# Kernel tuning notes

Measured on AMD Instinct MI355X. Metric: run time of the kernel, lower is better.

Reference implementation:

```python
import jax, jax.numpy as jnp
import numpy as np

H = 16  # n_heads (from init_kwargs)


def l2norm(x, eps=1e-6):
    return x * jax.lax.rsqrt(jnp.sum(x * x, axis=-1, keepdims=True) + eps)


def causal_conv1d(x, w, b):
    # depthwise causal conv: x (B,T,D), w (D,k), b (D,). Matches torch
    # Conv1d(d,d,k,groups=d,padding=k-1) followed by [:, :, :T] truncation.
    T = x.shape[1]
    k = w.shape[1]
    xp = jnp.pad(x, ((0, 0), (k - 1, 0), (0, 0)))
    y = b
    for j in range(k):  # k=4 taps, fixed small loop
        y = y + xp[:, j:j + T, :] * w[:, j]
    return y


def setup_inputs():
    key = jax.random.key(0)
    ks = jax.random.split(key, 16)
    B, T, D, kc = 2, 2048, 1024, 4
    d = D // H
    s = 1.0 / np.sqrt(D)
    return {
        "x": jax.random.normal(ks[0], (B, T, D), jnp.float32),
        "Wq": jax.random.normal(ks[1], (D, D), jnp.float32) * s,
        "Wk": jax.random.normal(ks[2], (D, D), jnp.float32) * s,
        "Wv": jax.random.normal(ks[3], (D, D), jnp.float32) * s,
        "Wo": jax.random.normal(ks[4], (D, D), jnp.float32) * s,
        "Wg": jax.random.normal(ks[5], (D, D), jnp.float32) * s,
        "Wb": jax.random.normal(ks[6], (D, H), jnp.float32) * s,
        "cq_w": jax.random.normal(ks[7], (D, kc), jnp.float32) * 0.3,
        "cq_b": jax.random.normal(ks[8], (D,), jnp.float32) * 0.1,
        "ck_w": jax.random.normal(ks[9], (D, kc), jnp.float32) * 0.3,
        "ck_b": jax.random.normal(ks[10], (D,), jnp.float32) * 0.1,
        "cv_w": jax.random.normal(ks[11], (D, kc), jnp.float32) * 0.3,
        "cv_b": jax.random.normal(ks[12], (D,), jnp.float32) * 0.1,
        "nw": jnp.ones((d,), jnp.float32),
    }


def reference(x, Wq, Wk, Wv, Wo, Wg, Wb, cq_w, cq_b, ck_w, ck_b, cv_w, cv_b, nw):
    B, T, D = x.shape
    d = D // H
    q = l2norm(jax.nn.silu(causal_conv1d(x @ Wq, cq_w, cq_b)).reshape(B, T, H, d))
    q = q / jnp.sqrt(jnp.asarray(d, x.dtype))
    k = l2norm(jax.nn.silu(causal_conv1d(x @ Wk, ck_w, ck_b)).reshape(B, T, H, d))
    v = jax.nn.silu(causal_conv1d(x @ Wv, cv_w, cv_b)).reshape(B, T, H, d)
    gate = (x @ Wg).reshape(B, T, H, d)
    beta = jax.nn.sigmoid(x @ Wb)[..., None]  # (B,T,H,1)

    def step(S, qkvb):
        q_t, k_t, v_t, b_t = qkvb  # (B,H,d), (B,H,d), (B,H,d), (B,H,1)
        err = (v_t - jnp.einsum('bhk,bhkv->bhv', k_t, S)) * b_t
        S = S + jnp.einsum('bhk,bhv->bhkv', k_t, err)
        o_t = jnp.einsum('bhk,bhkv->bhv', q_t, S)
        return S, o_t

    S0 = jnp.zeros((B, H, d, d), x.dtype)
    xs = (q.transpose(1, 0, 2, 3), k.transpose(1, 0, 2, 3),
          v.transpose(1, 0, 2, 3), beta.transpose(1, 0, 2, 3))
    _, oT = jax.lax.scan(step, S0, xs)
    o = oT.transpose(1, 0, 2, 3)  # (B,T,H,d)
    # RMSNorm over head_dim
    o = o * jax.lax.rsqrt(jnp.mean(o * o, axis=-1, keepdims=True) + 1e-5) * nw
    o = o * jax.nn.silu(gate)
    return o.reshape(B, T, D) @ Wo
```

## Files before the change

### kernel.cpp

```cpp
#include <hip/hip_runtime.h>
#include <hip/hip_bf16.h>

typedef __attribute__((ext_vector_type(8))) short short8;
typedef __attribute__((ext_vector_type(4))) float f32x4;

#define TSEQ 2048
#define DMODEL 1024
#define NH 16
#define HD 64
#define PLANE 4194304

__device__ __forceinline__ ushort f2bf(float f) {
    union { float f; unsigned int u; } c; c.f = f;
    unsigned int u = c.u + 0x7fffu + ((c.u >> 16) & 1u);
    return (ushort)(u >> 16);
}

__device__ __forceinline__ float bf2f(ushort u) {
    union { unsigned int i; float f; } c; c.i = ((unsigned int)u) << 16;
    return c.f;
}

__device__ __forceinline__ void split2(float x, ushort& h, ushort& l) {
    h = f2bf(x);
    float r = x - bf2f(h);
    l = f2bf(r);
}

__device__ __forceinline__ float silu_f(float y) {
    return y / (1.f + __expf(-y));
}

__device__ __forceinline__ void gl_lds16(const float* g, float* l) {
    __builtin_amdgcn_global_load_lds(
        (__attribute__((address_space(1))) void*)g,
        (__attribute__((address_space(3))) void*)l, 16, 0, 0);
}
__device__ __forceinline__ void gl_lds16u(const ushort* g, ushort* l) {
    __builtin_amdgcn_global_load_lds(
        (__attribute__((address_space(1))) void*)g,
        (__attribute__((address_space(3))) void*)l, 16, 0, 0);
}

__global__ void gdn_cvt_x(const float* __restrict__ x, ushort* __restrict__ xb) {
    int i = blockIdx.x * 256 + threadIdx.x;
    float4 v = ((const float4*)x)[i];
    ushort4 o;
    o.x = f2bf(v.x); o.y = f2bf(v.y); o.z = f2bf(v.z); o.w = f2bf(v.w);
    ((ushort4*)xb)[i] = o;
}

__global__ void gdn_cvt_w(const float* __restrict__ Wq, const float* __restrict__ Wk,
                          const float* __restrict__ Wv, const float* __restrict__ Wg,
                          const float* __restrict__ Wo, ushort* __restrict__ wt) {
    __shared__ float tile[32][33];
    int z = blockIdx.z;
    const float* W = (z == 0) ? Wq : (z == 1) ? Wk : (z == 2) ? Wv : (z == 3) ? Wg : Wo;
    int n0 = blockIdx.x * 32, k0 = blockIdx.y * 32;
    int tx = threadIdx.x, ty = threadIdx.y;
    #pragma unroll
    for (int j = 0; j < 32; j += 8)
        tile[ty + j][tx] = W[(size_t)(k0 + ty + j) * DMODEL + n0 + tx];
    __syncthreads();
    ushort* o = wt + (size_t)z * DMODEL * DMODEL;
    #pragma unroll
    for (int j = 0; j < 32; j += 8)
        o[(size_t)(n0 + ty + j) * DMODEL + k0 + tx] = f2bf(tile[tx][ty + j]);
}

__global__ void gdn_beta(const float* __restrict__ x, const float* __restrict__ Wb,
                         float* __restrict__ betaT) {
    __shared__ float xs[16][DMODEL];
    int tid = threadIdx.x;
    int m0 = blockIdx.x * 16;
    #pragma unroll
    for (int i = 0; i < 16; i++) {
        int idx = i * 256 + tid;
        int row = idx >> 8, c4 = idx & 255;
        *(float4*)&xs[row][c4 * 4] =
            *(const float4*)&x[(size_t)(m0 + row) * DMODEL + c4 * 4];
    }
    __syncthreads();
    int h = tid & 15, mi = tid >> 4;
    float acc = 0.f;
    for (int k = 0; k < DMODEL; ++k)
        acc += xs[mi][k] * Wb[k * NH + h];
    int m = m0 + mi;
    int b = m >> 11, t = m & (TSEQ - 1);
    betaT[((b * NH + h) << 11) + t] = 1.f / (1.f + __expf(-acc));
}

#define BK 32
__global__ __launch_bounds__(256) void gdn_gemm(const ushort* __restrict__ A,
                                                const ushort* __restrict__ Bt,
                                                float* __restrict__ outF,
                                                size_t planeStride) {
    __shared__ ushort As[128 * BK];
    __shared__ ushort Bs[128 * BK];
    int tid = threadIdx.x;
    int lane = tid & 63, wid = tid >> 6;
    int wm = wid & 1, wn = wid >> 1;
    int l15 = lane & 15, quad = lane >> 4;
    int bm = blockIdx.x, bn = blockIdx.y;
    const int K = DMODEL;

    int e0 = wid, e1 = wid + 4;
    int srow0 = e0 * 16 + (lane >> 2), srow1 = e1 * 16 + (lane >> 2);
    int scol = (lane & 3) * 8;
    const ushort* Ag0 = A + (size_t)(bm * 128 + srow0) * K + scol;
    const ushort* Ag1 = A + (size_t)(bm * 128 + srow1) * K + scol;
    const ushort* Bg0 = Bt + (size_t)(bn * 128 + srow0) * K + scol;
    const ushort* Bg1 = Bt + (size_t)(bn * 128 + srow1) * K + scol;
    ushort* Al0 = As + e0 * 512;
    ushort* Al1 = As + e1 * 512;
    ushort* Bl0 = Bs + e0 * 512;
    ushort* Bl1 = Bs + e1 * 512;

    f32x4 acc[4][4];
    #pragma unroll
    for (int i = 0; i < 4; i++)
        #pragma unroll
        for (int j = 0; j < 4; j++)
            acc[i][j] = (f32x4){0.f, 0.f, 0.f, 0.f};

    for (int kt = 0; kt < K; kt += BK) {
        __syncthreads();
        gl_lds16u(Ag0 + kt, Al0);
        gl_lds16u(Ag1 + kt, Al1);
        gl_lds16u(Bg0 + kt, Bl0);
        gl_lds16u(Bg1 + kt, Bl1);
        __syncthreads();
        short8 af[4], bf[4];
        #pragma unroll
        for (int i = 0; i < 4; i++) {
            af[i] = *(const short8*)&As[(wm * 64 + i * 16 + l15) * BK + quad * 8];
            bf[i] = *(const short8*)&Bs[(wn * 64 + i * 16 + l15) * BK + quad * 8];
        }
        #pragma unroll
        for (int mt = 0; mt < 4; mt++)
            #pragma unroll
            for (int nt = 0; nt < 4; nt++)
                acc[mt][nt] = __builtin_amdgcn_mfma_f32_16x16x32_bf16(
                    af[mt], bf[nt], acc[mt][nt], 0, 0, 0);
    }

    #pragma unroll
    for (int mt = 0; mt < 4; mt++)
        #pragma unroll
        for (int nt = 0; nt < 4; nt++)
            #pragma unroll
            for (int r = 0; r < 4; r++) {
                int row = bm * 128 + wm * 64 + mt * 16 + quad * 4 + r;
                int col = bn * 128 + wn * 64 + nt * 16 + l15;
                outF[(size_t)(col >> 10) * planeStride + (size_t)row * 1024 + (col & 1023)]
                    = acc[mt][nt][r];
            }
}

__global__ __launch_bounds__(512, 2) void gdn_gemm256(const ushort* __restrict__ A,
                                                      const ushort* __restrict__ Bt,
                                                      float* __restrict__ outF,
                                                      size_t planeStride) {
    __shared__ ushort As[3][256 * BK];
    __shared__ ushort Bs[3][256 * BK];
    int tid = threadIdx.x;
    int lane = tid & 63, wid = tid >> 6;
    int wm = wid >> 2, wn = wid & 3;
    int l15 = lane & 15, quad = lane >> 4;
    int bm = blockIdx.x, bn = blockIdx.y;
    const int K = DMODEL;

    int e0 = wid * 2, e1 = wid * 2 + 1;
    int srow0 = e0 * 16 + (lane >> 2), srow1 = e1 * 16 + (lane >> 2);
    int scol = (lane & 3) * 8;
    const ushort* Ag0 = A + (size_t)(bm * 256 + srow0) * K + scol;
    const ushort* Ag1 = A + (size_t)(bm * 256 + srow1) * K + scol;
    const ushort* Bg0 = Bt + (size_t)(bn * 256 + srow0) * K + scol;
    const ushort* Bg1 = Bt + (size_t)(bn * 256 + srow1) * K + scol;

    f32x4 acc[8][4];
    #pragma unroll
    for (int i = 0; i < 8; i++)
        #pragma unroll
        for (int j = 0; j < 4; j++)
            acc[i][j] = (f32x4){0.f, 0.f, 0.f, 0.f};

    #pragma unroll
    for (int t = 0; t < 2; t++) {
        gl_lds16u(Ag0 + t * BK, &As[t][e0 * 512]);
        gl_lds16u(Ag1 + t * BK, &As[t][e1 * 512]);
        gl_lds16u(Bg0 + t * BK, &Bs[t][e0 * 512]);
        gl_lds16u(Bg1 + t * BK, &Bs[t][e1 * 512]);
    }
    asm volatile("s_waitcnt vmcnt(4)" ::: "memory");
    __builtin_amdgcn_s_barrier();

    #pragma unroll 1
    for (int c = 0; c < 32; ++c) {
        if (c + 2 < 32) {
            int s2 = (c + 2) % 3;
            int kt2 = (c + 2) * BK;
            gl_lds16u(Ag0 + kt2, &As[s2][e0 * 512]);
            gl_lds16u(Ag1 + kt2, &As[s2][e1 * 512]);
            gl_lds16u(Bg0 + kt2, &Bs[s2][e0 * 512]);
            gl_lds16u(Bg1 + kt2, &Bs[s2][e1 * 512]);
        }
        int cs = c % 3;
        short8 af[8], bf[4];
        #pragma unroll
        for (int mi = 0; mi < 8; mi++)
            af[mi] = *(const short8*)&As[cs][(wm * 128 + mi * 16 + l15) * BK + quad * 8];
        #pragma unroll
        for (int ni = 0; ni < 4; ni++)
            bf[ni] = *(const short8*)&Bs[cs][(wn * 64 + ni * 16 + l15) * BK + quad * 8];
        #pragma unroll
        for (int mi = 0; mi < 8; mi++)
            #pragma unroll
            for (int ni = 0; ni < 4; ni++)
                acc[mi][ni] = __builtin_amdgcn_mfma_f32_16x16x32_bf16(
                    af[mi], bf[ni], acc[mi][ni], 0, 0, 0);
        if (c < 30) {
            asm volatile("s_waitcnt vmcnt(4)" ::: "memory");
            __builtin_amdgcn_s_barrier();
        } else if (c == 30) {
            asm volatile("s_waitcnt vmcnt(0)" ::: "memory");
            __builtin_amdgcn_s_barrier();
        }
    }

    #pragma unroll
    for (int mi = 0; mi < 8; mi++)
        #pragma unroll
        for (int ni = 0; ni < 4; ni++)
            #pragma unroll
            for (int r = 0; r < 4; r++) {
                int row = bm * 256 + wm * 128 + mi * 16 + quad * 4 + r;
                int col = bn * 256 + wn * 64 + ni * 16 + l15;
                outF[(size_t)(col >> 10) * planeStride + (size_t)row * 1024 + (col & 1023)]
                    = acc[mi][ni][r];
            }
}

__global__ void gdn_conv(const float* __restrict__ pre,
                         const float* __restrict__ cqw, const float* __restrict__ cqb,
                         const float* __restrict__ ckw, const float* __restrict__ ckb,
                         const float* __restrict__ cvw, const float* __restrict__ cvb,
                         float* __restrict__ qn, float* __restrict__ kn, float* __restrict__ vn) {
    int m = blockIdx.x;
    int which = blockIdx.y;
    int t = m & (TSEQ - 1);
    const float* cw = (which == 0) ? cqw : (which == 1) ? ckw : cvw;
    const float* cb = (which == 0) ? cqb : (which == 1) ? ckb : cvb;
    float* dst = (which == 0) ? qn : (which == 1) ? kn : vn;
    int c = threadIdx.x * 4;

    float w[4][4];
    #pragma unroll
    for (int i = 0; i < 4; i++) {
        float4 t4 = ((const float4*)cw)[c + i];
        w[i][0] = t4.x; w[i][1] = t4.y; w[i][2] = t4.z; w[i][3] = t4.w;
    }
    float4 bias = ((const float4*)cb)[threadIdx.x];
    float y[4] = {bias.x, bias.y, bias.z, bias.w};

    const float* src = pre + (size_t)which * PLANE + (size_t)m * DMODEL + c;
    #pragma unroll
    for (int j = 0; j < 4; j++) {
        int tt = t - 3 + j;
        if (tt >= 0) {
            float4 xv = *(const float4*)(src + (long)(j - 3) * DMODEL);
            y[0] += xv.x * w[0][j];
            y[1] += xv.y * w[1][j];
            y[2] += xv.z * w[2][j];
            y[3] += xv.w * w[3][j];
        }
    }
    #pragma unroll
    for (int i = 0; i < 4; i++) y[i] = silu_f(y[i]);

    if (which < 2) {
        float ss = y[0]*y[0] + y[1]*y[1] + y[2]*y[2] + y[3]*y[3];
        ss += __shfl_xor(ss, 1);
        ss += __shfl_xor(ss, 2);
        ss += __shfl_xor(ss, 4);
        ss += __shfl_xor(ss, 8);
        float sc = rsqrtf(ss + 1e-6f);
        if (which == 0) sc *= 0.125f;
        #pragma unroll
        for (int i = 0; i < 4; i++) y[i] *= sc;
    }
    float4 o; o.x = y[0]; o.y = y[1]; o.z = y[2]; o.w = y[3];
    ((float4*)(dst + (size_t)m * 1024))[threadIdx.x] = o;
}

__global__ __launch_bounds__(256) void gdn_chunk(
    const float* __restrict__ kn, const float* __restrict__ vn,
    const float* __restrict__ betaT,
    ushort* __restrict__ WTst, ushort* __restrict__ U0st,
    float* __restrict__ Pst, float* __restrict__ Rst)
{
    __shared__ ushort Khi[64 * 72], Klo[64 * 72];
    __shared__ ushort KThi[64 * 72], KTlo[64 * 72];
    __shared__ ushort XThi[128 * 72], XTlo[128 * 72];
    __shared__ ushort Mneghi[64 * 72], Mneglo[64 * 72];
    __shared__ float  Xf[64 * 132];
    __shared__ float  MmDiag[4 * 16 * 20];
    __shared__ float  bet[64];

    int c = blockIdx.x, bh = blockIdx.y;
    int b = bh >> 4, h = bh & 15;
    int tid = threadIdx.x;
    int w = tid >> 6, lane = tid & 63;
    int l15 = lane & 15, quad = lane >> 4;
    size_t gbase = ((size_t)(b * TSEQ + c * 64)) * DMODEL + h * 64;
    size_t u = (size_t)bh * 32 + c;

    if (tid < 64) bet[tid] = betaT[((size_t)bh << 11) + c * 64 + tid];
    #pragma unroll
    for (int i = 0; i < 18; i++) {
        ((uint*)XThi)[tid + 256 * i] = 0u;
        ((uint*)XTlo)[tid + 256 * i] = 0u;
    }
    __syncthreads();

    #pragma unroll
    for (int i = 0; i < 4; i++) {
        int idx = tid + 256 * i;
        int r = idx >> 4, c4 = (idx & 15) * 4;
        float4 kv = *(const float4*)&kn[gbase + (size_t)r * DMODEL + c4];
        float4 vv = *(const float4*)&vn[gbase + (size_t)r * DMODEL + c4];
        float br = bet[r];
        float4 xk; xk.x = br * kv.x; xk.y = br * kv.y; xk.z = br * kv.z; xk.w = br * kv.w;
        float4 xv; xv.x = br * vv.x; xv.y = br * vv.y; xv.z = br * vv.z; xv.w = br * vv.w;
        *(float4*)&Xf[r * 132 + c4] = xk;
        *(float4*)&Xf[r * 132 + 64 + c4] = xv;
        ushort h0, l0, h1, l1, h2, l2, h3, l3;
        split2(kv.x, h0, l0); split2(kv.y, h1, l1);
        split2(kv.z, h2, l2); split2(kv.w, h3, l3);
        ((uint*)&Khi[r * 72 + c4])[0] = (uint)h0 | ((uint)h1 << 16);
        ((uint*)&Khi[r * 72 + c4])[1] = (uint)h2 | ((uint)h3 << 16);
        ((uint*)&Klo[r * 72 + c4])[0] = (uint)l0 | ((uint)l1 << 16);
        ((uint*)&Klo[r * 72 + c4])[1] = (uint)l2 | ((uint)l3 << 16);
        KThi[(c4 + 0) * 72 + r] = h0; KThi[(c4 + 1) * 72 + r] = h1;
        KThi[(c4 + 2) * 72 + r] = h2; KThi[(c4 + 3) * 72 + r] = h3;
        KTlo[(c4 + 0) * 72 + r] = l0; KTlo[(c4 + 1) * 72 + r] = l1;
        KTlo[(c4 + 2) * 72 + r] = l2; KTlo[(c4 + 3) * 72 + r] = l3;
    }
    __syncthreads();

    {
        f32x4 mAcc[4];
        #pragma unroll
        for (int tn = 0; tn < 4; tn++) mAcc[tn] = (f32x4){0.f, 0.f, 0.f, 0.f};
        #pragma unroll
        for (int ks = 0; ks < 2; ks++) {
            short8 aH = *(const short8*)&Khi[(16 * w + l15) * 72 + ks * 32 + quad * 8];
            short8 aL = *(const short8*)&Klo[(16 * w + l15) * 72 + ks * 32 + quad * 8];
            #pragma unroll
            for (int tn = 0; tn < 4; tn++) {
                short8 bH = *(const short8*)&Khi[(16 * tn + l15) * 72 + ks * 32 + quad * 8];
                short8 bL = *(const short8*)&Klo[(16 * tn + l15) * 72 + ks * 32 + quad * 8];
                mAcc[tn] = __builtin_amdgcn_mfma_f32_16x16x32_bf16(aH, bH, mAcc[tn], 0, 0, 0);
                mAcc[tn] = __builtin_amdgcn_mfma_f32_16x16x32_bf16(aH, bL, mAcc[tn], 0, 0, 0);
                mAcc[tn] = __builtin_amdgcn_mfma_f32_16x16x32_bf16(aL, bH, mAcc[tn], 0, 0, 0);
            }
        }
        #pragma unroll
        for (int tn = 0; tn < 4; tn++) {
            #pragma unroll
            for (int r = 0; r < 4; r++) {
                int row = 16 * w + quad * 4 + r;
                int col = tn * 16 + l15;
                float val = mAcc[tn][r] * bet[row];
                ushort hh = 0, ll = 0;
                if (col < row) {
                    float nv = -val;
                    hh = f2bf(nv);
                    ll = f2bf(nv - bf2f(hh));
                }
                Mneghi[row * 72 + col] = hh;
                Mneglo[row * 72 + col] = ll;
                if (tn == w) MmDiag[w * 320 + (row & 15) * 20 + l15] = val;
            }
        }
    }
    __syncthreads();

    #pragma unroll 1
    for (int st = 0; st < 4; st++) {
        int tb = st * 16;
        if (st) {
            f32x4 acc2[2];
            #pragma unroll
            for (int e = 0; e < 2; e++) {
                int tn = 2 * w + e;
                #pragma unroll
                for (int r = 0; r < 4; r++)
                    acc2[e][r] = Xf[(tb + quad * 4 + r) * 132 + tn * 16 + l15];
            }
            #pragma unroll
            for (int ks = 0; ks < 2; ks++) {
                short8 aH = *(const short8*)&Mneghi[(tb + l15) * 72 + ks * 32 + quad * 8];
                short8 aL = *(const short8*)&Mneglo[(tb + l15) * 72 + ks * 32 + quad * 8];
                #pragma unroll
                for (int e = 0; e < 2; e++) {
                    int tn = 2 * w + e;
                    short8 bH = *(const short8*)&XThi[(tn * 16 + l15) * 72 + ks * 32 + quad * 8];
                    short8 bL = *(const short8*)&XTlo[(tn * 16 + l15) * 72 + ks * 32 + quad * 8];
                    acc2[e] = __builtin_amdgcn_mfma_f32_16x16x32_bf16(aH, bH, acc2[e], 0, 0, 0);
                    acc2[e] = __builtin_amdgcn_mfma_f32_16x16x32_bf16(aH, bL, acc2[e], 0, 0, 0);
                    acc2[e] = __builtin_amdgcn_mfma_f32_16x16x32_bf16(aL, bH, acc2[e], 0, 0, 0);
                }
            }
            #pragma unroll
            for (int e = 0; e < 2; e++) {
                int tn = 2 * w + e;
                #pragma unroll
                for (int r = 0; r < 4; r++)
                    Xf[(tb + quad * 4 + r) * 132 + tn * 16 + l15] = acc2[e][r];
            }
        }
        __syncthreads();

        if (tid < 128) {
            const int j = tid;
            const float* MD = &MmDiag[st * 320];
            float xr[16];
            #pragma unroll
            for (int sb = 0; sb < 4; sb++) {
                float b4[4];
                #pragma unroll
                for (int i = 0; i < 4; i++)
                    b4[i] = Xf[(tb + sb * 4 + i) * 132 + j];
                #pragma unroll
                for (int u4 = 0; u4 < sb; u4++) {
                    #pragma unroll
                    for (int i = 0; i < 4; i++) {
                        float4 m4 = *(const float4*)&MD[(sb * 4 + i) * 20 + u4 * 4];
                        b4[i] -= m4.x * xr[u4 * 4 + 0] + m4.y * xr[u4 * 4 + 1]
                               + m4.z * xr[u4 * 4 + 2] + m4.w * xr[u4 * 4 + 3];
                    }
                }
                float x0 = b4[0];
                float x1 = b4[1] - MD[(sb * 4 + 1) * 20 + sb * 4 + 0] * x0;
                float x2 = b4[2] - MD[(sb * 4 + 2) * 20 + sb * 4 + 0] * x0
                                 - MD[(sb * 4 + 2) * 20 + sb * 4 + 1] * x1;
                float x3 = b4[3] - MD[(sb * 4 + 3) * 20 + sb * 4 + 0] * x0
                                 - MD[(sb * 4 + 3) * 20 + sb * 4 + 1] * x1
                                 - MD[(sb * 4 + 3) * 20 + sb * 4 + 2] * x2;
                xr[sb * 4 + 0] = x0; xr[sb * 4 + 1] = x1;
                xr[sb * 4 + 2] = x2; xr[sb * 4 + 3] = x3;
            }
            ushort hs[16], ls[16];
            #pragma unroll
            for (int i = 0; i < 16; i++) split2(xr[i], hs[i], ls[i]);
            uint4 ph0, ph1, pl0, pl1;
            ph0.x = (uint)hs[0] | ((uint)hs[1] << 16);  ph0.y = (uint)hs[2] | ((uint)hs[3] << 16);
            ph0.z = (uint)hs[4] | ((uint)hs[5] << 16);  ph0.w = (uint)hs[6] | ((uint)hs[7] << 16);
            ph1.x = (uint)hs[8] | ((uint)hs[9] << 16);  ph1.y = (uint)hs[10] | ((uint)hs[11] << 16);
            ph1.z = (uint)hs[12] | ((uint)hs[13] << 16); ph1.w = (uint)hs[14] | ((uint)hs[15] << 16);
            pl0.x = (uint)ls[0] | ((uint)ls[1] << 16);  pl0.y = (uint)ls[2] | ((uint)ls[3] << 16);
            pl0.z = (uint)ls[4] | ((uint)ls[5] << 16);  pl0.w = (uint)ls[6] | ((uint)ls[7] << 16);
            pl1.x = (uint)ls[8] | ((uint)ls[9] << 16);  pl1.y = (uint)ls[10] | ((uint)ls[11] << 16);
            pl1.z = (uint)ls[12] | ((uint)ls[13] << 16); pl1.w = (uint)ls[14] | ((uint)ls[15] << 16);
            *(uint4*)&XThi[j * 72 + tb] = ph0;  *(uint4*)&XThi[j * 72 + tb + 8] = ph1;
            *(uint4*)&XTlo[j * 72 + tb] = pl0;  *(uint4*)&XTlo[j * 72 + tb + 8] = pl1;
            if (j < 64) {
                ushort* wdst = WTst + u * 4096 + j * 64 + tb;
                *(uint4*)wdst = ph0; *(uint4*)(wdst + 8) = ph1;
            } else {
                ushort* udst = U0st + u * 4096 + (size_t)tb * 64 + (j - 64);
                #pragma unroll
                for (int i = 0; i < 16; i++) udst[i * 64] = hs[i];
            }
        }
        __syncthreads();
    }

    {
        f32x4 pAcc[4], rAcc[4];
        #pragma unroll
        for (int tn = 0; tn < 4; tn++) {
            pAcc[tn] = (f32x4){0.f, 0.f, 0.f, 0.f};
            rAcc[tn] = (f32x4){0.f, 0.f, 0.f, 0.f};
        }
        #pragma unroll
        for (int ks = 0; ks < 2; ks++) {
            short8 aH = *(const short8*)&XThi[(16 * w + l15) * 72 + ks * 32 + quad * 8];
            short8 aL = *(const short8*)&XTlo[(16 * w + l15) * 72 + ks * 32 + quad * 8];
            short8 cH = *(const short8*)&KThi[(16 * w + l15) * 72 + ks * 32 + quad * 8];
            short8 cL = *(const short8*)&KTlo[(16 * w + l15) * 72 + ks * 32 + quad * 8];
            #pragma unroll
            for (int tn = 0; tn < 4; tn++) {
                short8 bH = *(const short8*)&KThi[(16 * tn + l15) * 72 + ks * 32 + quad * 8];
                short8 bL = *(const short8*)&KTlo[(16 * tn + l15) * 72 + ks * 32 + quad * 8];
                pAcc[tn] = __builtin_amdgcn_mfma_f32_16x16x32_bf16(aH, bH, pAcc[tn], 0, 0, 0);
                pAcc[tn] = __builtin_amdgcn_mfma_f32_16x16x32_bf16(aH, bL, pAcc[tn], 0, 0, 0);
                pAcc[tn] = __builtin_amdgcn_mfma_f32_16x16x32_bf16(aL, bH, pAcc[tn], 0, 0, 0);
                short8 uH = *(const short8*)&XThi[(64 + 16 * tn + l15) * 72 + ks * 32 + quad * 8];
                short8 uL = *(const short8*)&XTlo[(64 + 16 * tn + l15) * 72 + ks * 32 + quad * 8];
                rAcc[tn] = __builtin_amdgcn_mfma_f32_16x16x32_bf16(cH, uH, rAcc[tn], 0, 0, 0);
                rAcc[tn] = __builtin_amdgcn_mfma_f32_16x16x32_bf16(cH, uL, rAcc[tn], 0, 0, 0);
                rAcc[tn] = __builtin_amdgcn_mfma_f32_16x16x32_bf16(cL, uH, rAcc[tn], 0, 0, 0);
            }
        }
        float* Po = Pst + u * 4096;
        float* Ro = Rst + u * 4096;
        #pragma unroll
        for (int tn = 0; tn < 4; tn++) {
            #pragma unroll
            for (int r = 0; r < 4; r++) {
                int row = 16 * w + quad * 4 + r;
                int col = tn * 16 + l15;
                Po[row * 64 + col] = pAcc[tn][r];
                Ro[col * 64 + row] = rAcc[tn][r];
            }
        }
    }
}

__global__ __launch_bounds__(256) void gdn_sstep(const float* __restrict__ Pst,
                                                 const float* __restrict__ Rst,
                                                 float* __restrict__ S0st)
{
    __shared__ float PTl[3][4096];
    __shared__ float Rl[3][1024];
    __shared__ float SshT[2][16][72];

    int bh = blockIdx.x >> 2, cg = blockIdx.x & 3;
    int tid = threadIdx.x;
    int t0 = (tid & 15) * 4;
    int j  = tid >> 4;
    int jg = cg * 16 + j;
    int wv = tid >> 6, ln = tid & 63;

    size_t ubase = (size_t)bh * 32 * 4096;

    *(float4*)&SshT[0][j][t0] = (float4){0.f, 0.f, 0.f, 0.f};

    #pragma unroll
    for (int t = 0; t < 2; t++) {
        size_t ub = ubase + (size_t)t * 4096;
        #pragma unroll
        for (int q = 0; q < 4; q++)
            gl_lds16(Pst + ub + (wv * 4 + q) * 256 + ln * 4, &PTl[t][(wv * 4 + q) * 256]);
        gl_lds16(Rst + ub + cg * 1024 + wv * 256 + ln * 4, &Rl[t][wv * 256]);
    }
    asm volatile("s_waitcnt vmcnt(5)" ::: "memory");
    asm volatile("s_waitcnt lgkmcnt(0)" ::: "memory");
    __builtin_amdgcn_s_barrier();

    int cur3 = 0;
    #pragma unroll 1
    for (int c = 0; c < 32; ++c) {
        int cur = c & 1, nxt = cur ^ 1;
        if (c + 2 < 32) {
            int b3 = cur3 + 2; if (b3 >= 3) b3 -= 3;
            size_t ub2 = ubase + (size_t)(c + 2) * 4096;
            #pragma unroll
            for (int q = 0; q < 4; q++)
                gl_lds16(Pst + ub2 + (wv * 4 + q) * 256 + ln * 4, &PTl[b3][(wv * 4 + q) * 256]);
            gl_lds16(Rst + ub2 + cg * 1024 + wv * 256 + ln * 4, &Rl[b3][wv * 256]);
        }
        float4 sold = *(const float4*)&SshT[cur][j][t0];
        size_t ub = ubase + (size_t)c * 4096;
        S0st[ub + (size_t)(t0 + 0) * 64 + jg] = sold.x;
        S0st[ub + (size_t)(t0 + 1) * 64 + jg] = sold.y;
        S0st[ub + (size_t)(t0 + 2) * 64 + jg] = sold.z;
        S0st[ub + (size_t)(t0 + 3) * 64 + jg] = sold.w;
        float4 racc = *(const float4*)&Rl[cur3][j * 64 + t0];
        float sub0 = 0.f, sub1 = 0.f, sub2 = 0.f, sub3 = 0.f;
        #pragma unroll
        for (int u4 = 0; u4 < 16; u4++) {
            float4 sv = *(const float4*)&SshT[cur][j][u4 * 4];
            #pragma unroll
            for (int e = 0; e < 4; e++) {
                float4 pt = *(const float4*)&PTl[cur3][(u4 * 4 + e) * 64 + t0];
                float s1 = (e == 0) ? sv.x : (e == 1) ? sv.y : (e == 2) ? sv.z : sv.w;
                sub0 = fmaf(pt.x, s1, sub0);
                sub1 = fmaf(pt.y, s1, sub1);
                sub2 = fmaf(pt.z, s1, sub2);
                sub3 = fmaf(pt.w, s1, sub3);
            }
        }
        float4 snew;
        snew.x = sold.x + racc.x - sub0;
        snew.y = sold.y + racc.y - sub1;
        snew.z = sold.z + racc.z - sub2;
        snew.w = sold.w + racc.w - sub3;
        *(float4*)&SshT[nxt][j][t0] = snew;
        if (c == 0)       { asm volatile("s_waitcnt vmcnt(9)"  ::: "memory"); }
        else if (c < 30)  { asm volatile("s_waitcnt vmcnt(13)" ::: "memory"); }
        else if (c == 30) { asm volatile("s_waitcnt vmcnt(8)"  ::: "memory"); }
        asm volatile("s_waitcnt lgkmcnt(0)" ::: "memory");
        __builtin_amdgcn_s_barrier();
        cur3 += 1; if (cur3 >= 3) cur3 -= 3;
    }
}

__global__ __launch_bounds__(256) void gdn_opass(
    const float* __restrict__ qn, const float* __restrict__ kn,
    const float* __restrict__ S0st, const ushort* __restrict__ WTst,
    const ushort* __restrict__ U0st, float* __restrict__ otmp2)
{
    __shared__ ushort pool[36864];
    ushort* Qhi  = pool;
    ushort* Qlo  = pool + 4608;
    ushort* Khi  = pool + 2 * 4608;
    ushort* Klo  = pool + 3 * 4608;
    ushort* SThi = pool + 4 * 4608;
    ushort* STlo = pool + 5 * 4608;
    ushort* Wn   = pool + 6 * 4608;
    ushort* Uu   = pool + 7 * 4608;
    ushort* Ghi  = Qhi;  ushort* Glo  = Qlo;
    ushort* EThi = Khi;  ushort* ETlo = Klo;

    int c = blockIdx.x, bh = blockIdx.y;
    int b = bh >> 4, h = bh & 15;
    int tid = threadIdx.x;
    int w = tid >> 6, lane = tid & 63;
    int l15 = lane & 15, quad = lane >> 4;
    size_t gbase = ((size_t)(b * TSEQ + c * 64)) * DMODEL + h * 64;
    size_t u = (size_t)bh * 32 + c;

    #pragma unroll
    for (int i = 0; i < 4; i++) {
        int idx = tid + 256 * i;
        int r = idx >> 4, c4 = (idx & 15) * 4;
        float4 qv = *(const float4*)&qn[gbase + (size_t)r * DMODEL + c4];
        float4 kv = *(const float4*)&kn[gbase + (size_t)r * DMODEL + c4];
        float4 sv = *(const float4*)&S0st[u * 4096 + (size_t)idx * 4];
        ushort h0, l0, h1, l1, h2, l2, h3, l3;
        split2(qv.x, h0, l0); split2(qv.y, h1, l1);
        split2(qv.z, h2, l2); split2(qv.w, h3, l3);
        ((uint*)&Qhi[r * 72 + c4])[0] = (uint)h0 | ((uint)h1 << 16);
        ((uint*)&Qhi[r * 72 + c4])[1] = (uint)h2 | ((uint)h3 << 16);
        ((uint*)&Qlo[r * 72 + c4])[0] = (uint)l0 | ((uint)l1 << 16);
        ((uint*)&Qlo[r * 72 + c4])[1] = (uint)l2 | ((uint)l3 << 16);
        split2(kv.x, h0, l0); split2(kv.y, h1, l1);
        split2(kv.z, h2, l2); split2(kv.w, h3, l3);
        ((uint*)&Khi[r * 72 + c4])[0] = (uint)h0 | ((uint)h1 << 16);
        ((uint*)&Khi[r * 72 + c4])[1] = (uint)h2 | ((uint)h3 << 16);
        ((uint*)&Klo[r * 72 + c4])[0] = (uint)l0 | ((uint)l1 << 16);
        ((uint*)&Klo[r * 72 + c4])[1] = (uint)l2 | ((uint)l3 << 16);
        split2(sv.x, h0, l0); split2(sv.y, h1, l1);
        split2(sv.z, h2, l2); split2(sv.w, h3, l3);
        SThi[(c4 + 0) * 72 + r] = h0; STlo[(c4 + 0) * 72 + r] = l0;
        SThi[(c4 + 1) * 72 + r] = h1; STlo[(c4 + 1) * 72 + r] = l1;
        SThi[(c4 + 2) * 72 + r] = h2; STlo[(c4 + 2) * 72 + r] = l2;
        SThi[(c4 + 3) * 72 + r] = h3; STlo[(c4 + 3) * 72 + r] = l3;
    }
    #pragma unroll
    for (int i = 0; i < 2; i++) {
        int idx = tid + 256 * i;
        uint4 w8 = ((const uint4*)(WTst + u * 4096))[idx];
        int ur = idx >> 3, t8 = (idx & 7) * 8;
        uint v0 = w8.x ^ 0x80008000u, v1 = w8.y ^ 0x80008000u;
        uint v2 = w8.z ^ 0x80008000u, v3 = w8.w ^ 0x80008000u;
        Wn[(t8 + 0) * 72 + ur] = (ushort)v0; Wn[(t8 + 1) * 72 + ur] = (ushort)(v0 >> 16);
        Wn[(t8 + 2) * 72 + ur] = (ushort)v1; Wn[(t8 + 3) * 72 + ur] = (ushort)(v1 >> 16);
        Wn[(t8 + 4) * 72 + ur] = (ushort)v2; Wn[(t8 + 5) * 72 + ur] = (ushort)(v2 >> 16);
        Wn[(t8 + 6) * 72 + ur] = (ushort)v3; Wn[(t8 + 7) * 72 + ur] = (ushort)(v3 >> 16);
        ((uint4*)Uu)[idx] = ((const uint4*)(U0st + u * 4096))[idx];
    }
    __syncthreads();

    f32x4 accG[4], accO[4], accE[4];
    #pragma unroll
    for (int tn = 0; tn < 4; tn++) {
        accG[tn] = (f32x4){0.f, 0.f, 0.f, 0.f};
        accO[tn] = (f32x4){0.f, 0.f, 0.f, 0.f};
        #pragma unroll
        for (int r = 0; r < 4; r++)
            accE[tn][r] = bf2f(Uu[(16 * w + quad * 4 + r) * 64 + tn * 16 + l15]);
    }
    #pragma unroll
    for (int ks = 0; ks < 2; ks++) {
        int ko = ks * 32 + quad * 8;
        short8 qH = *(const short8*)&Qhi[(16 * w + l15) * 72 + ko];
        short8 qL = *(const short8*)&Qlo[(16 * w + l15) * 72 + ko];
        short8 wA = *(const short8*)&Wn [(16 * w + l15) * 72 + ko];
        #pragma unroll
        for (int tn = 0; tn < 4; tn++) {
            short8 kH = *(const short8*)&Khi [(16 * tn + l15) * 72 + ko];
            short8 kL = *(const short8*)&Klo [(16 * tn + l15) * 72 + ko];
            short8 sH = *(const short8*)&SThi[(16 * tn + l15) * 72 + ko];
            short8 sL = *(const short8*)&STlo[(16 * tn + l15) * 72 + ko];
            accG[tn] = __builtin_amdgcn_mfma_f32_16x16x32_bf16(qH, kH, accG[tn], 0, 0, 0);
            accG[tn] = __builtin_amdgcn_mfma_f32_16x16x32_bf16(qH, kL, accG[tn], 0, 0, 0);
            accG[tn] = __builtin_amdgcn_mfma_f32_16x16x32_bf16(qL, kH, accG[tn], 0, 0, 0);
            accO[tn] = __builtin_amdgcn_mfma_f32_16x16x32_bf16(qH, sH, accO[tn], 0, 0, 0);
            accO[tn] = __builtin_amdgcn_mfma_f32_16x16x32_bf16(qH, sL, accO[tn], 0, 0, 0);
            accO[tn] = __builtin_amdgcn_mfma_f32_16x16x32_bf16(qL, sH, accO[tn], 0, 0, 0);
            accE[tn] = __builtin_amdgcn_mfma_f32_16x16x32_bf16(wA, sH, accE[tn], 0, 0, 0);
            accE[tn] = __builtin_amdgcn_mfma_f32_16x16x32_bf16(wA, sL, accE[tn], 0, 0, 0);
        }
    }
    __syncthreads();

    #pragma unroll
    for (int tn = 0; tn < 4; tn++) {
        #pragma unroll
        for (int r = 0; r < 4; r++) {
            int row = 16 * w + quad * 4 + r;
            int col = tn * 16 + l15;
            float gv = (col <= row) ? accG[tn][r] : 0.f;
            ushort gh, gl; split2(gv, gh, gl);
            Ghi[row * 72 + col] = gh; Glo[row * 72 + col] = gl;
            ushort eh, el; split2(accE[tn][r], eh, el);
            EThi[col * 72 + row] = eh; ETlo[col * 72 + row] = el;
        }
    }
    __syncthreads();

    #pragma unroll
    for (int ks = 0; ks < 2; ks++) {
        int ko = ks * 32 + quad * 8;
        short8 gH = *(const short8*)&Ghi[(16 * w + l15) * 72 + ko];
        short8 gL = *(const short8*)&Glo[(16 * w + l15) * 72 + ko];
        #pragma unroll
        for (int tn = 0; tn < 4; tn++) {
            short8 eH = *(const short8*)&EThi[(16 * tn + l15) * 72 + ko];
            short8 eL = *(const short8*)&ETlo[(16 * tn + l15) * 72 + ko];
            accO[tn] = __builtin_amdgcn_mfma_f32_16x16x32_bf16(gH, eH, accO[tn], 0, 0, 0);
            accO[tn] = __builtin_amdgcn_mfma_f32_16x16x32_bf16(gH, eL, accO[tn], 0, 0, 0);
            accO[tn] = __builtin_amdgcn_mfma_f32_16x16x32_bf16(gL, eH, accO[tn], 0, 0, 0);
        }
    }

    #pragma unroll
    for (int tn = 0; tn < 4; tn++) {
        #pragma unroll
        for (int r = 0; r < 4; r++) {
            int row = 16 * w + quad * 4 + r;
            int col = tn * 16 + l15;
            otmp2[(((size_t)bh * 16 + (col >> 2)) * TSEQ + c * 64 + row) * 4 + (col & 3)]
                = accO[tn][r];
        }
    }
}

__global__ void gdn_fuse(const float* __restrict__ otmp2, const float* __restrict__ pre,
                         const float* __restrict__ nw, ushort* __restrict__ ofused) {
    int m = blockIdx.x;
    int b = m >> 11, t = m & (TSEQ - 1);
    int tid = threadIdx.x;
    float4 o = ((const float4*)otmp2)[((size_t)((b * NH + (tid >> 4)) * 16 + (tid & 15))) * TSEQ + t];
    float ss = o.x*o.x + o.y*o.y + o.z*o.z + o.w*o.w;
    ss += __shfl_xor(ss, 1);
    ss += __shfl_xor(ss, 2);
    ss += __shfl_xor(ss, 4);
    ss += __shfl_xor(ss, 8);
    float r = rsqrtf(ss * (1.f / 64.f) + 1e-5f);
    float4 nwv = ((const float4*)nw)[tid & 15];
    float4 g = ((const float4*)(pre + 3 * (size_t)PLANE + (size_t)m * DMODEL))[tid];
    ushort4 out;
    out.x = f2bf(o.x * r * nwv.x * silu_f(g.x));
    out.y = f2bf(o.y * r * nwv.y * silu_f(g.y));
    out.z = f2bf(o.z * r * nwv.z * silu_f(g.z));
    out.w = f2bf(o.w * r * nwv.w * silu_f(g.w));
    ((ushort4*)ofused)[m * 256 + tid] = out;
}

extern "C" void kernel_launch(void* const* d_in, const int* in_sizes, int n_in,
                              void* d_out, int out_size, void* d_ws, size_t ws_size,
                              hipStream_t stream) {
    const float* x    = (const float*)d_in[0];
    const float* Wq   = (const float*)d_in[1];
    const float* Wk   = (const float*)d_in[2];
    const float* Wv   = (const float*)d_in[3];
    const float* Wo   = (const float*)d_in[4];
    const float* Wg   = (const float*)d_in[5];
    const float* Wb   = (const float*)d_in[6];
    const float* cq_w = (const float*)d_in[7];
    const float* cq_b = (const float*)d_in[8];
    const float* ck_w = (const float*)d_in[9];
    const float* ck_b = (const float*)d_in[10];
    const float* cv_w = (const float*)d_in[11];
    const float* cv_b = (const float*)d_in[12];
    const float* nw   = (const float*)d_in[13];

    char* ws = (char*)d_ws;
    ushort* xb     = (ushort*)(ws);
    ushort* wt     = (ushort*)(ws + 8388608);
    float*  pre    = (float*)(ws + 18874368);
    float*  qn     = (float*)(ws + 85983232);
    float*  kn     = (float*)(ws + 102760448);
    float*  vn     = (float*)(ws + 119537664);
    float*  betaT  = (float*)(ws + 136314880);
    float*  otmp2  = (float*)(ws + 136577024);
    ushort* ofused = (ushort*)(ws + 153354240);

    float*  Pst  = pre;
    float*  Rst  = pre + PLANE;
    float*  S0st = pre + 2 * PLANE;
    ushort* WTst = xb;
    ushort* U0st = ofused;

    gdn_cvt_x<<<4096, 256, 0, stream>>>(x, xb);
    gdn_cvt_w<<<dim3(32, 32, 5), dim3(32, 8), 0, stream>>>(Wq, Wk, Wv, Wg, Wo, wt);
    gdn_beta<<<256, 256, 0, stream>>>(x, Wb, betaT);
    gdn_gemm256<<<dim3(16, 16), 512, 0, stream>>>(xb, wt, pre, (size_t)PLANE);
    gdn_conv<<<dim3(4096, 3), 256, 0, stream>>>(pre, cq_w, cq_b, ck_w, ck_b, cv_w, cv_b,
                                                qn, kn, vn);
    gdn_chunk<<<dim3(32, 32), 256, 0, stream>>>(kn, vn, betaT, WTst, U0st, Pst, Rst);
    gdn_sstep<<<128, 256, 0, stream>>>(Pst, Rst, S0st);
    gdn_opass<<<dim3(32, 32), 256, 0, stream>>>(qn, kn, S0st, WTst, U0st, otmp2);
    gdn_fuse<<<4096, 256, 0, stream>>>(otmp2, pre, nw, ofused);
    gdn_gemm<<<dim3(32, 8), 256, 0, stream>>>(ofused, wt + 4 * 1024 * 1024,
                                              (float*)d_out, (size_t)0);
}
```

Measured before the change: 393.2 us.

## Alias shared buffers in gdn_chunk to cut LDS and raise occupancy

Reorganises shared memory in the chunk kernel so K and the negated M matrix share one buffer, while K-transpose, the per-subtile X staging and the diagonal blocks share another. The X buffer is shrunk to a 16-row slice loaded from global memory at each substep, and K-transpose is rebuilt from global after the solve. Launch bounds request two blocks per CU. This is meant to lower LDS use so more blocks fit per CU. The cost is extra global reloads of k and v, plus additional barriers.

Result: faster. 375.5 us (-4.5%).

```diff
diff --git a/kernel.cpp b/kernel.cpp
--- a/kernel.cpp
+++ b/kernel.cpp
@@ -293,19 +293,23 @@
     ((float4*)(dst + (size_t)m * 1024))[threadIdx.x] = o;
 }
 
-__global__ __launch_bounds__(256) void gdn_chunk(
+__global__ __launch_bounds__(256, 2) void gdn_chunk(
     const float* __restrict__ kn, const float* __restrict__ vn,
     const float* __restrict__ betaT,
     ushort* __restrict__ WTst, ushort* __restrict__ U0st,
     float* __restrict__ Pst, float* __restrict__ Rst)
 {
-    __shared__ ushort Khi[64 * 72], Klo[64 * 72];
-    __shared__ ushort KThi[64 * 72], KTlo[64 * 72];
-    __shared__ ushort XThi[128 * 72], XTlo[128 * 72];
-    __shared__ ushort Mneghi[64 * 72], Mneglo[64 * 72];
-    __shared__ float  Xf[64 * 132];
-    __shared__ float  MmDiag[4 * 16 * 20];
-    __shared__ float  bet[64];
+    __shared__ __align__(16) ushort bufA[2 * 4608];
+    __shared__ __align__(16) ushort bufKT[2 * 4608];
+    __shared__ __align__(16) ushort XThi[128 * 72];
+    __shared__ __align__(16) ushort XTlo[128 * 72];
+    __shared__ float bet[64];
+
+    ushort* Khi    = bufA;          ushort* Klo    = bufA + 4608;
+    ushort* Mneghi = bufA;          ushort* Mneglo = bufA + 4608;
+    ushort* KThi   = bufKT;         ushort* KTlo   = bufKT + 4608;
+    float*  Xs     = (float*)bufKT;
+    float*  MmDiag = (float*)(bufKT + 4608);
 
     int c = blockIdx.x, bh = blockIdx.y;
     int b = bh >> 4, h = bh & 15;
@@ -321,19 +325,11 @@
         ((uint*)XThi)[tid + 256 * i] = 0u;
         ((uint*)XTlo)[tid + 256 * i] = 0u;
     }
-    __syncthreads();
-
     #pragma unroll
     for (int i = 0; i < 4; i++) {
         int idx = tid + 256 * i;
         int r = idx >> 4, c4 = (idx & 15) * 4;
         float4 kv = *(const float4*)&kn[gbase + (size_t)r * DMODEL + c4];
-        float4 vv = *(const float4*)&vn[gbase + (size_t)r * DMODEL + c4];
-        float br = bet[r];
-        float4 xk; xk.x = br * kv.x; xk.y = br * kv.y; xk.z = br * kv.z; xk.w = br * kv.w;
-        float4 xv; xv.x = br * vv.x; xv.y = br * vv.y; xv.z = br * vv.z; xv.w = br * vv.w;
-        *(float4*)&Xf[r * 132 + c4] = xk;
-        *(float4*)&Xf[r * 132 + 64 + c4] = xv;
         ushort h0, l0, h1, l1, h2, l2, h3, l3;
         split2(kv.x, h0, l0); split2(kv.y, h1, l1);
         split2(kv.z, h2, l2); split2(kv.w, h3, l3);
@@ -341,10 +337,6 @@
         ((uint*)&Khi[r * 72 + c4])[1] = (uint)h2 | ((uint)h3 << 16);
         ((uint*)&Klo[r * 72 + c4])[0] = (uint)l0 | ((uint)l1 << 16);
         ((uint*)&Klo[r * 72 + c4])[1] = (uint)l2 | ((uint)l3 << 16);
-        KThi[(c4 + 0) * 72 + r] = h0; KThi[(c4 + 1) * 72 + r] = h1;
-        KThi[(c4 + 2) * 72 + r] = h2; KThi[(c4 + 3) * 72 + r] = h3;
-        KTlo[(c4 + 0) * 72 + r] = l0; KTlo[(c4 + 1) * 72 + r] = l1;
-        KTlo[(c4 + 2) * 72 + r] = l2; KTlo[(c4 + 3) * 72 + r] = l3;
     }
     __syncthreads();
 
@@ -365,6 +357,7 @@
                 mAcc[tn] = __builtin_amdgcn_mfma_f32_16x16x32_bf16(aL, bH, mAcc[tn], 0, 0, 0);
             }
         }
+        __syncthreads();
         #pragma unroll
         for (int tn = 0; tn < 4; tn++) {
             #pragma unroll
@@ -389,6 +382,19 @@
     #pragma unroll 1
     for (int st = 0; st < 4; st++) {
         int tb = st * 16;
+        {
+            int rl = tid >> 4, c4 = (tid & 15) * 4;
+            int r = tb + rl;
+            float br = bet[r];
+            float4 kv = *(const float4*)&kn[gbase + (size_t)r * DMODEL + c4];
+            float4 vv = *(const float4*)&vn[gbase + (size_t)r * DMODEL + c4];
+            float4 xk; xk.x = br * kv.x; xk.y = br * kv.y; xk.z = br * kv.z; xk.w = br * kv.w;
+            float4 xv; xv.x = br * vv.x; xv.y = br * vv.y; xv.z = br * vv.z; xv.w = br * vv.w;
+            *(float4*)&Xs[rl * 132 + c4] = xk;
+            *(float4*)&Xs[rl * 132 + 64 + c4] = xv;
+        }
+        __syncthreads();
+
         if (st) {
             f32x4 acc2[2];
             #pragma unroll
@@ -396,7 +402,7 @@
                 int tn = 2 * w + e;
                 #pragma unroll
                 for (int r = 0; r < 4; r++)
-                    acc2[e][r] = Xf[(tb + quad * 4 + r) * 132 + tn * 16 + l15];
+                    acc2[e][r] = Xs[(quad * 4 + r) * 132 + tn * 16 + l15];
             }
             #pragma unroll
             for (int ks = 0; ks < 2; ks++) {
@@ -417,10 +423,10 @@
                 int tn = 2 * w + e;
                 #pragma unroll
                 for (int r = 0; r < 4; r++)
-                    Xf[(tb + quad * 4 + r) * 132 + tn * 16 + l15] = acc2[e][r];
-            }
-        }
-        __syncthreads();
+                    Xs[(quad * 4 + r) * 132 + tn * 16 + l15] = acc2[e][r];
+            }
+            __syncthreads();
+        }
 
         if (tid < 128) {
             const int j = tid;
@@ -431,7 +437,7 @@
                 float b4[4];
                 #pragma unroll
                 for (int i = 0; i < 4; i++)
-                    b4[i] = Xf[(tb + sb * 4 + i) * 132 + j];
+                    b4[i] = Xs[(sb * 4 + i) * 132 + j];
                 #pragma unroll
                 for (int u4 = 0; u4 < sb; u4++) {
                     #pragma unroll
@@ -476,6 +482,21 @@
         }
         __syncthreads();
     }
+
+    #pragma unroll
+    for (int i = 0; i < 4; i++) {
+        int idx = tid + 256 * i;
+        int r = idx >> 4, c4 = (idx & 15) * 4;
+        float4 kv = *(const float4*)&kn[gbase + (size_t)r * DMODEL + c4];
+        ushort h0, l0, h1, l1, h2, l2, h3, l3;
+        split2(kv.x, h0, l0); split2(kv.y, h1, l1);
+        split2(kv.z, h2, l2); split2(kv.w, h3, l3);
+        KThi[(c4 + 0) * 72 + r] = h0; KThi[(c4 + 1) * 72 + r] = h1;
+        KThi[(c4 + 2) * 72 + r] = h2; KThi[(c4 + 3) * 72 + r] = h3;
+        KTlo[(c4 + 0) * 72 + r] = l0; KTlo[(c4 + 1) * 72 + r] = l1;
+        KTlo[(c4 + 2) * 72 + r] = l2; KTlo[(c4 + 3) * 72 + r] = l3;
+    }
+    __syncthreads();
 
     {
         f32x4 pAcc[4], rAcc[4];
```
